# Performance work log

Measured on AMD Instinct MI355X. Metric: run time of the kernel, lower is better.

Reference implementation:

```python
import jax, jax.numpy as jnp
import numpy as np

FRAMES_IN = 5   # SAMPLING_INPUT_FRAMES = 50 // 10
FRAMES_OUT = 3  # SAMPLING_OUTPUT_FRAMES = 30 // 10
T, N, F, C, H = 512, 60, 2, 64, 512  # trajectories, nodes, features, gcn out, lstm hidden
DIST_THRESH = 10.0
EXIST_THRESH = 0.04


def setup_inputs() -> dict:
    key = jax.random.key(0)
    ks = jax.random.split(key, 24)
    p = {}
    p["feature_input"] = jax.random.normal(ks[0], (FRAMES_IN, T * N, F), jnp.float32)
    p["adj"] = jax.random.randint(ks[1], (FRAMES_IN, T, N, N), 0, 2).astype(jnp.float32)
    p["std"] = jax.random.uniform(ks[2], (F,), jnp.float32)
    p["mean"] = jax.random.normal(ks[3], (F,), jnp.float32)
    # GCNConv params
    p["gcn_W"] = jax.random.normal(ks[4], (F, C), jnp.float32) / np.sqrt(F)
    p["gcn_b"] = jnp.zeros((C,), jnp.float32)
    # LSTM params (PyTorch layout: gates i,f,g,o stacked)
    In = C * N
    s = 1.0 / np.sqrt(H)
    p["W_ih"] = jax.random.uniform(ks[5], (4 * H, In), jnp.float32, -s, s)
    p["W_hh"] = jax.random.uniform(ks[6], (4 * H, H), jnp.float32, -s, s)
    p["b_ih"] = jax.random.uniform(ks[7], (4 * H,), jnp.float32, -s, s)
    p["b_hh"] = jax.random.uniform(ks[8], (4 * H,), jnp.float32, -s, s)
    # MLP: H->512->1028->512->F*N
    def lin(k, fi, fo):
        b = 1.0 / np.sqrt(fi)
        return jax.random.uniform(k, (fi, fo), jnp.float32, -b, b)
    p["W1"] = lin(ks[9], H, 512); p["b1"] = jnp.zeros((512,), jnp.float32)
    p["W2"] = lin(ks[10], 512, 1028); p["b2"] = jnp.zeros((1028,), jnp.float32)
    p["W3"] = lin(ks[11], 1028, 512); p["b3"] = jnp.zeros((512,), jnp.float32)
    p["W4"] = lin(ks[12], 512, F * N); p["b4"] = jnp.zeros((F * N,), jnp.float32)
    return p


def _gcn(x_flat, adjf, gcn_W, gcn_b):
    # x_flat: [T*N, F]; adjf: [T, N, N] block-diagonal graph per trajectory
    x = x_flat.reshape(T, N, F)
    A = adjf + jnp.eye(N, dtype=adjf.dtype)  # PyG GCNConv adds self-loops on top
    deg = A.sum(-1)                            # [T, N]
    norm = jnp.where(deg > 0, jax.lax.rsqrt(deg), 0.0)
    h = x @ gcn_W                              # [T, N, C]
    out = norm[..., None] * jnp.einsum('tij,tjc->tic', A, norm[..., None] * h) + gcn_b
    return out.reshape(T, N * C)


def _lstm(x, h, c, W_ih, W_hh, b_ih, b_hh):
    gates = x @ W_ih.T + b_ih + h @ W_hh.T + b_hh
    i, f, g, o = jnp.split(gates, 4, axis=-1)
    c = jax.nn.sigmoid(f) * c + jax.nn.sigmoid(i) * jnp.tanh(g)
    h = jax.nn.sigmoid(o) * jnp.tanh(c)
    return h, c


def _mlp(h, W1, b1, W2, b2, W3, b3, W4, b4):
    h = jax.nn.relu(h @ W1 + b1)
    h = jax.nn.relu(h @ W2 + b2)
    h = jax.nn.relu(h @ W3 + b3)
    return h @ W4 + b4  # [T, F*N]


def _find_adj(pred, std, mean):
    # radius-graph construction (denormalized coords, block per trajectory)
    x = jax.lax.stop_gradient(pred * std + mean).reshape(T, N, F)
    exist = (x[..., 0] > EXIST_THRESH) & (x[..., 1] > EXIST_THRESH)  # [T, N]
    diff = x[:, :, None, :2] - x[:, None, :, :2]
    dist = jnp.sqrt(jnp.sum(diff * diff, -1))                        # [T, N, N]
    eye = jnp.eye(N, dtype=bool)
    conn = ((dist > 0) & (dist < DIST_THRESH)) | eye
    adj = exist[:, :, None] & exist[:, None, :] & conn
    return adj.astype(pred.dtype)


def reference(feature_input, adj, std, mean, gcn_W, gcn_b, W_ih, W_hh, b_ih, b_hh,
              W1, b1, W2, b2, W3, b3, W4, b4):
    h = jnp.zeros((T, H), feature_input.dtype)
    c = jnp.zeros((T, H), feature_input.dtype)
    enc = [feature_input[0]]
    for i in range(FRAMES_IN - 1):  # break at last frame in original
        g = _gcn(feature_input[i], adj[i], gcn_W, gcn_b)
        h, c = _lstm(g, h, c, W_ih, W_hh, b_ih, b_hh)
        pred = _mlp(h, W1, b1, W2, b2, W3, b3, W4, b4).reshape(T * N, F)
        enc.append(pred)
    cur_x, cur_adj = feature_input[FRAMES_IN - 1], adj[FRAMES_IN - 1]
    dec = []
    for _ in range(FRAMES_OUT):
        g = _gcn(cur_x, cur_adj, gcn_W, gcn_b)
        h, c = _lstm(g, h, c, W_ih, W_hh, b_ih, b_hh)
        pred = _mlp(h, W1, b1, W2, b2, W3, b3, W4, b4).reshape(T * N, F)
        dec.append(pred)
        cur_x = pred
        cur_adj = _find_adj(pred, std, mean)
    return jnp.stack(enc), jnp.stack(dec)
```

## Files before the change

### kernel.cpp

```cpp
#include <hip/hip_runtime.h>

#define T_ 512
#define N_ 60
#define F_ 2
#define C_ 64
#define H_ 512
#define IN_ 3840
#define FOURH 2048
#define PRED_SZ 61440
#define ADJ_SZ 1843200
#define K2_ 128
#define LDSK 40
#define HSLOT 262144

typedef __attribute__((ext_vector_type(8))) short bf8;
typedef __attribute__((ext_vector_type(4))) float f4;

__device__ __forceinline__ unsigned short f2bf(float f)
{
    unsigned int u = __float_as_uint(f);
    u = (u + 0x7FFFu + ((u >> 16) & 1u)) >> 16;
    return (unsigned short)u;
}

__global__ void prep_init_k(const float* Whh, const float* W1, const float* W2,
                            const float* W3, const float* W4, const float* feat,
                            unsigned short* Whh_bf, unsigned short* W1_bf,
                            unsigned short* W2_bf, unsigned short* W3_bf,
                            unsigned short* W4_bf,
                            unsigned short* hAll, float* c, float* out)
{
    long i = (long)blockIdx.x * 256 + threadIdx.x;
    if (i < 1048576) { Whh_bf[i] = f2bf(Whh[i]); return; }
    i -= 1048576;
    if (i < 262144) { W1_bf[i] = f2bf(W1[i]); return; }
    i -= 262144;
    if (i < 526336) { W2_bf[i] = f2bf(W2[i]); return; }
    i -= 526336;
    if (i < 526336) { W3_bf[i] = f2bf(W3[i]); return; }
    i -= 526336;
    if (i < 61440) { W4_bf[i] = f2bf(W4[i]); return; }
    i -= 61440;
    hAll[i] = 0;
    c[i] = 0.0f;
    if (i < PRED_SZ) out[i] = feat[i];
}

__global__ __launch_bounds__(256) void wih2_k(
    const float* Wih, const float* W, const float* b,
    const float* bih, const float* bhh,
    unsigned short* Wih2_bf, float* biasAll)
{
    __shared__ float row[IN_];
    __shared__ float wc[2][64];
    __shared__ float bb[64];
    __shared__ float red[256];

    int o = blockIdx.x;
    int tid = threadIdx.x;

    if (tid < 128) wc[tid >> 6][tid & 63] = W[tid];
    if (tid < 64) bb[tid] = b[tid];
    for (int k = tid; k < IN_; k += 256) row[k] = Wih[(long)o * IN_ + k];
    __syncthreads();

    if (tid < 128) {
        float s = 0.0f;
        if (tid < 120) {
            int n = tid >> 1;
            int f = tid & 1;
            for (int c2 = 0; c2 < 64; ++c2) s += row[n * 64 + c2] * wc[f][c2];
        }
        Wih2_bf[(long)o * K2_ + tid] = f2bf(s);
    }

    float sb = 0.0f;
    for (int k = tid; k < IN_; k += 256) sb += row[k] * bb[k & 63];
    red[tid] = sb;
    __syncthreads();
    for (int s = 128; s > 0; s >>= 1) {
        if (tid < s) red[tid] += red[tid + s];
        __syncthreads();
    }
    if (tid == 0) biasAll[o] = bih[o] + bhh[o] + red[0];
}

__global__ __launch_bounds__(128) void gcn_enc_y(
    const float* x, const float* adj, unsigned short* Y)
{
    __shared__ float sA[N_][N_];
    __shared__ float sx[N_][2];
    __shared__ float snorm[N_];

    int frame = blockIdx.x >> 9;
    int t = blockIdx.x & 511;
    const float* xf = x + (long)frame * PRED_SZ + (long)t * 120;
    const float* af = adj + (long)frame * ADJ_SZ + (long)t * 3600;
    int tid = threadIdx.x;

    for (int l = tid; l < N_ * N_; l += 128) {
        int i = l / N_;
        int j = l - i * N_;
        float a = af[l];
        if (i == j) a += 1.0f;
        sA[i][j] = a;
    }
    if (tid < 120) sx[tid >> 1][tid & 1] = xf[tid];
    __syncthreads();

    if (tid < N_) {
        float d = 0.0f;
        for (int j = 0; j < N_; ++j) d += sA[tid][j];
        snorm[tid] = (d > 0.0f) ? rsqrtf(d) : 0.0f;
    }
    __syncthreads();

    if (tid < 128) {
        float y = 0.0f;
        if (tid < 120) {
            int n = tid >> 1;
            int f = tid & 1;
            float s = 0.0f;
            for (int j = 0; j < N_; ++j) s += sA[n][j] * snorm[j] * sx[j][f];
            y = snorm[n] * s;
        }
        Y[(long)blockIdx.x * K2_ + tid] = f2bf(y);
    }
}

__global__ __launch_bounds__(128) void gcn_dec_y(
    const float* pred, const float* stdv, const float* meanv, unsigned short* Y)
{
    __shared__ float sA[N_][N_];
    __shared__ float sx[N_][2];
    __shared__ float dx0[N_];
    __shared__ float dx1[N_];
    __shared__ int sex[N_];
    __shared__ float snorm[N_];

    int t = blockIdx.x;
    int tid = threadIdx.x;
    const float* pr = pred + (long)t * 120;

    if (tid < 120) sx[tid >> 1][tid & 1] = pr[tid];
    if (tid < N_) {
        float vx = pr[tid * 2 + 0] * stdv[0] + meanv[0];
        float vy = pr[tid * 2 + 1] * stdv[1] + meanv[1];
        dx0[tid] = vx;
        dx1[tid] = vy;
        sex[tid] = (vx > 0.04f) && (vy > 0.04f);
    }
    __syncthreads();

    for (int l = tid; l < N_ * N_; l += 128) {
        int i = l / N_;
        int j = l - i * N_;
        float ddx = dx0[i] - dx0[j];
        float ddy = dx1[i] - dx1[j];
        float d = sqrtf(ddx * ddx + ddy * ddy);
        int conn = ((d > 0.0f) && (d < 10.0f)) || (i == j);
        float a = (sex[i] && sex[j] && conn) ? 1.0f : 0.0f;
        if (i == j) a += 1.0f;
        sA[i][j] = a;
    }
    __syncthreads();

    if (tid < N_) {
        float d = 0.0f;
        for (int j = 0; j < N_; ++j) d += sA[tid][j];
        snorm[tid] = (d > 0.0f) ? rsqrtf(d) : 0.0f;
    }
    __syncthreads();

    if (tid < 128) {
        float y = 0.0f;
        if (tid < 120) {
            int n = tid >> 1;
            int f = tid & 1;
            float s = 0.0f;
            for (int j = 0; j < N_; ++j) s += sA[n][j] * snorm[j] * sx[j][f];
            y = snorm[n] * s;
        }
        Y[(long)t * K2_ + tid] = f2bf(y);
    }
}

__global__ __launch_bounds__(256) void mlp_gemm(
    const unsigned short* Abf, const unsigned short* Bb,
    const float* bias1, float* Cf, unsigned short* Cbf,
    int M, int Nc, int K, int mode)
{
    __shared__ unsigned short As[2][32 * LDSK];
    __shared__ unsigned short Bs[2][32 * LDSK];

    int tid = threadIdx.x;
    int wave = tid >> 6;
    int wt = wave >> 1, wj = wave & 1;
    int lane = tid & 63;
    int quad = lane >> 4;
    int l16 = lane & 15;
    int row0 = blockIdx.y * 32;
    int col0 = blockIdx.x * 32;

    f4 acc = {0.f, 0.f, 0.f, 0.f};
    const ushort4 zu = make_ushort4(0, 0, 0, 0);

    int sr = tid >> 3;
    int sko = (tid & 7) * 4;

    auto loadA = [&](int k0, ushort4& v) {
        int gm = row0 + sr, gk = k0 + sko;
        v = zu;
        if (gm < M && gk + 4 <= K) v = *(const ushort4*)&Abf[(long)gm * K + gk];
    };
    auto loadB = [&](int k0, ushort4& v) {
        int gk = k0 + sr;
        int gn0 = col0 + sko;
        v = zu;
        if (gk < K) {
            if (gn0 + 4 <= Nc) {
                v = *(const ushort4*)&Bb[(long)gk * Nc + gn0];
            } else {
                unsigned short tmp[4] = {0, 0, 0, 0};
                for (int i = 0; i < 4; ++i)
                    if (gn0 + i < Nc) tmp[i] = Bb[(long)gk * Nc + gn0 + i];
                v = make_ushort4(tmp[0], tmp[1], tmp[2], tmp[3]);
            }
        }
    };

    int niter = (K + 31) / 32;
    ushort4 a0, b0, a1 = zu, b1 = zu, a2 = zu, b2 = zu;
    loadA(0, a0);
    loadB(0, b0);
    if (niter > 1) { loadA(32, a1); loadB(32, b1); }

    for (int it = 0; it < niter; ++it) {
        if (it + 2 < niter) {
            loadA((it + 2) * 32, a2);
            loadB((it + 2) * 32, b2);
        }
        int bf = it & 1;
        *(ushort4*)&As[bf][sr * LDSK + sko] = a0;
        Bs[bf][(sko + 0) * LDSK + sr] = b0.x;
        Bs[bf][(sko + 1) * LDSK + sr] = b0.y;
        Bs[bf][(sko + 2) * LDSK + sr] = b0.z;
        Bs[bf][(sko + 3) * LDSK + sr] = b0.w;
        __syncthreads();

        bf8 fa = *(const bf8*)&As[bf][(wt * 16 + l16) * LDSK + quad * 8];
        bf8 fb = *(const bf8*)&Bs[bf][(wj * 16 + l16) * LDSK + quad * 8];
        acc = __builtin_amdgcn_mfma_f32_16x16x32_bf16(fa, fb, acc, 0, 0, 0);

        a0 = a1; a1 = a2; b0 = b1; b1 = b2;
    }

    int gn = col0 + wj * 16 + l16;
    if (gn < Nc) {
        float bsv = bias1[gn];
        #pragma unroll
        for (int r = 0; r < 4; ++r) {
            int gm = row0 + wt * 16 + quad * 4 + r;
            if (gm >= M) continue;
            float v = acc[r] + bsv;
            long idx = (long)gm * Nc + gn;
            if (mode == 2) {
                if (v < 0.0f) v = 0.0f;
                Cbf[idx] = f2bf(v);
            } else {
                Cf[idx] = v;
            }
        }
    }
}

__global__ __launch_bounds__(256) void mlp_w1b(
    const unsigned short* hAll, const unsigned short* Bb,
    const float* bias1, unsigned short* Cbf)
{
    __shared__ unsigned short As[2][32 * LDSK];
    __shared__ unsigned short Bs[2][32 * LDSK];

    int tid = threadIdx.x;
    int wave = tid >> 6;
    int wt = wave >> 1, wj = wave & 1;
    int lane = tid & 63;
    int quad = lane >> 4;
    int l16 = lane & 15;
    int row0 = blockIdx.y * 32;
    int col0 = blockIdx.x * 32;

    f4 acc = {0.f, 0.f, 0.f, 0.f};
    int sr = tid >> 3;
    int sko = (tid & 7) * 4;

    int gr = row0 + sr;
    int sidx = gr >> 9;
    int slot = (sidx < 4) ? (sidx + 1) : 7;
    const unsigned short* arow = hAll + (long)slot * HSLOT + (long)(gr & 511) * H_;

    auto loadA = [&](int k0, ushort4& v) {
        v = *(const ushort4*)&arow[k0 + sko];
    };
    auto loadB = [&](int k0, ushort4& v) {
        v = *(const ushort4*)&Bb[(long)(k0 + sr) * 512 + col0 + sko];
    };

    ushort4 a0, b0, a1, b1, a2 = make_ushort4(0,0,0,0), b2 = a2;
    loadA(0, a0); loadB(0, b0);
    loadA(32, a1); loadB(32, b1);

    for (int it = 0; it < 16; ++it) {
        if (it + 2 < 16) { loadA((it + 2) * 32, a2); loadB((it + 2) * 32, b2); }
        int bf = it & 1;
        *(ushort4*)&As[bf][sr * LDSK + sko] = a0;
        Bs[bf][(sko + 0) * LDSK + sr] = b0.x;
        Bs[bf][(sko + 1) * LDSK + sr] = b0.y;
        Bs[bf][(sko + 2) * LDSK + sr] = b0.z;
        Bs[bf][(sko + 3) * LDSK + sr] = b0.w;
        __syncthreads();

        bf8 fa = *(const bf8*)&As[bf][(wt * 16 + l16) * LDSK + quad * 8];
        bf8 fb = *(const bf8*)&Bs[bf][(wj * 16 + l16) * LDSK + quad * 8];
        acc = __builtin_amdgcn_mfma_f32_16x16x32_bf16(fa, fb, acc, 0, 0, 0);

        a0 = a1; a1 = a2; b0 = b1; b1 = b2;
    }

    int gn = col0 + wj * 16 + l16;
    float bsv = bias1[gn];
    #pragma unroll
    for (int r = 0; r < 4; ++r) {
        int gm = row0 + wt * 16 + quad * 4 + r;
        float v = acc[r] + bsv;
        if (v < 0.0f) v = 0.0f;
        Cbf[(long)gm * 512 + gn] = f2bf(v);
    }
}

__global__ __launch_bounds__(256) void mlp_w4b(
    const unsigned short* Abf, const unsigned short* Bb,
    const float* bias1, float* out)
{
    __shared__ unsigned short As[2][32 * LDSK];
    __shared__ unsigned short Bs[2][32 * LDSK];

    int tid = threadIdx.x;
    int wave = tid >> 6;
    int wt = wave >> 1, wj = wave & 1;
    int lane = tid & 63;
    int quad = lane >> 4;
    int l16 = lane & 15;
    int row0 = blockIdx.y * 32;
    int col0 = blockIdx.x * 32;

    f4 acc = {0.f, 0.f, 0.f, 0.f};
    const ushort4 zu = make_ushort4(0, 0, 0, 0);
    int sr = tid >> 3;
    int sko = (tid & 7) * 4;

    auto loadA = [&](int k0, ushort4& v) {
        v = *(const ushort4*)&Abf[(long)(row0 + sr) * 512 + k0 + sko];
    };
    auto loadB = [&](int k0, ushort4& v) {
        int gn0 = col0 + sko;
        v = zu;
        if (gn0 + 4 <= 120) {
            v = *(const ushort4*)&Bb[(long)(k0 + sr) * 120 + gn0];
        } else {
            unsigned short tmp[4] = {0, 0, 0, 0};
            for (int i = 0; i < 4; ++i)
                if (gn0 + i < 120) tmp[i] = Bb[(long)(k0 + sr) * 120 + gn0 + i];
            v = make_ushort4(tmp[0], tmp[1], tmp[2], tmp[3]);
        }
    };

    ushort4 a0, b0, a1, b1, a2 = zu, b2 = zu;
    loadA(0, a0); loadB(0, b0);
    loadA(32, a1); loadB(32, b1);

    for (int it = 0; it < 16; ++it) {
        if (it + 2 < 16) { loadA((it + 2) * 32, a2); loadB((it + 2) * 32, b2); }
        int bf = it & 1;
        *(ushort4*)&As[bf][sr * LDSK + sko] = a0;
        Bs[bf][(sko + 0) * LDSK + sr] = b0.x;
        Bs[bf][(sko + 1) * LDSK + sr] = b0.y;
        Bs[bf][(sko + 2) * LDSK + sr] = b0.z;
        Bs[bf][(sko + 3) * LDSK + sr] = b0.w;
        __syncthreads();

        bf8 fa = *(const bf8*)&As[bf][(wt * 16 + l16) * LDSK + quad * 8];
        bf8 fb = *(const bf8*)&Bs[bf][(wj * 16 + l16) * LDSK + quad * 8];
        acc = __builtin_amdgcn_mfma_f32_16x16x32_bf16(fa, fb, acc, 0, 0, 0);

        a0 = a1; a1 = a2; b0 = b1; b1 = b2;
    }

    int gn = col0 + wj * 16 + l16;
    if (gn < 120) {
        float bsv = bias1[gn];
        #pragma unroll
        for (int r = 0; r < 4; ++r) {
            int gm = row0 + wt * 16 + quad * 4 + r;
            int sidx = gm >> 9;
            int frame = (sidx < 4) ? (sidx + 1) : 7;
            out[(long)frame * PRED_SZ + (long)(gm & 511) * 120 + gn] = acc[r] + bsv;
        }
    }
}

__global__ __launch_bounds__(256) void whh_lstm_k(
    const unsigned short* hprev, const unsigned short* Whh_bf,
    const unsigned short* Yf, const unsigned short* Wih2_bf,
    const float* biasAll, float* c, unsigned short* hnew)
{
    __shared__ unsigned short As[2][32 * LDSK];
    __shared__ unsigned short Bs[2][128 * LDSK];

    int tid = threadIdx.x;
    int wave = tid >> 6;
    int wt = wave >> 1, wj = wave & 1;
    int lane = tid & 63;
    int quad = lane >> 4;
    int l16 = lane & 15;
    int j0 = blockIdx.x * 32;
    int row0 = blockIdx.y * 32;

    int sr = tid >> 3;
    int sko = (tid & 7) * 4;
    int br = tid >> 1;
    int bko = (tid & 1) * 16;
    long brow = (long)((br >> 5) * H_ + j0 + (br & 31));
    long bb_w = brow * H_;
    long bb_y = brow * K2_;
    long ar_h = (long)(row0 + sr) * H_;
    long ar_y = (long)(row0 + sr) * K2_;

    f4 acc[4];
    #pragma unroll
    for (int g = 0; g < 4; ++g) acc[g] = f4{0.f, 0.f, 0.f, 0.f};

    auto loadT = [&](int it, ushort4& a, uint4& q0, uint4& q1) {
        if (it < 4) {
            int k = it * 32;
            a  = *(const ushort4*)&Yf[ar_y + k + sko];
            q0 = *(const uint4*)&Wih2_bf[bb_y + k + bko];
            q1 = *(const uint4*)&Wih2_bf[bb_y + k + bko + 8];
        } else {
            int k = (it - 4) * 32;
            a  = *(const ushort4*)&hprev[ar_h + k + sko];
            q0 = *(const uint4*)&Whh_bf[bb_w + k + bko];
            q1 = *(const uint4*)&Whh_bf[bb_w + k + bko + 8];
        }
    };

    ushort4 a0, a1, a2 = make_ushort4(0, 0, 0, 0);
    uint4 q00, q01, q10, q11, q20 = uint4{0,0,0,0}, q21 = uint4{0,0,0,0};
    loadT(0, a0, q00, q01);
    loadT(1, a1, q10, q11);

    for (int it = 0; it < 20; ++it) {
        if (it + 2 < 20) loadT(it + 2, a2, q20, q21);
        int bf = it & 1;
        *(ushort4*)&As[bf][sr * LDSK + sko] = a0;
        *(uint4*)&Bs[bf][br * LDSK + bko]     = q00;
        *(uint4*)&Bs[bf][br * LDSK + bko + 8] = q01;
        __syncthreads();

        bf8 fa = *(const bf8*)&As[bf][(wt * 16 + l16) * LDSK + quad * 8];
        #pragma unroll
        for (int g = 0; g < 4; ++g) {
            bf8 fb = *(const bf8*)&Bs[bf][(g * 32 + wj * 16 + l16) * LDSK + quad * 8];
            acc[g] = __builtin_amdgcn_mfma_f32_16x16x32_bf16(fa, fb, acc[g], 0, 0, 0);
        }

        a0 = a1; a1 = a2;
        q00 = q10; q01 = q11; q10 = q20; q11 = q21;
    }

    int j = j0 + wj * 16 + l16;
    float b_i = biasAll[j];
    float b_f = biasAll[512 + j];
    float b_g = biasAll[1024 + j];
    float b_o = biasAll[1536 + j];
    #pragma unroll
    for (int r = 0; r < 4; ++r) {
        int t = row0 + wt * 16 + quad * 4 + r;
        float gi = acc[0][r] + b_i;
        float gf = acc[1][r] + b_f;
        float gg = acc[2][r] + b_g;
        float go = acc[3][r] + b_o;
        float ig = 1.0f / (1.0f + expf(-gi));
        float fg = 1.0f / (1.0f + expf(-gf));
        float g2 = tanhf(gg);
        float og = 1.0f / (1.0f + expf(-go));
        long ci = (long)t * H_ + j;
        float cn = fg * c[ci] + ig * g2;
        c[ci] = cn;
        hnew[ci] = f2bf(og * tanhf(cn));
    }
}

extern "C" void kernel_launch(void* const* d_in, const int* in_sizes, int n_in,
                              void* d_out, int out_size, void* d_ws, size_t ws_size,
                              hipStream_t stream)
{
    const float* feat  = (const float*)d_in[0];
    const float* adjin = (const float*)d_in[1];
    const float* stdv  = (const float*)d_in[2];
    const float* meanv = (const float*)d_in[3];
    const float* gcnW  = (const float*)d_in[4];
    const float* gcnb  = (const float*)d_in[5];
    const float* Wih   = (const float*)d_in[6];
    const float* Whh   = (const float*)d_in[7];
    const float* bih   = (const float*)d_in[8];
    const float* bhh   = (const float*)d_in[9];
    const float* W1    = (const float*)d_in[10];
    const float* b1    = (const float*)d_in[11];
    const float* W2    = (const float*)d_in[12];
    const float* b2    = (const float*)d_in[13];
    const float* W3    = (const float*)d_in[14];
    const float* b3    = (const float*)d_in[15];
    const float* W4    = (const float*)d_in[16];
    const float* b4    = (const float*)d_in[17];
    float* out = (float*)d_out;

    float* c       = (float*)d_ws;
    float* biasAll = c + 262144;
    unsigned short* Y       = (unsigned short*)(biasAll + 2048);
    unsigned short* hAll    = Y + 5 * 65536;
    unsigned short* m1      = hAll + 8 * HSLOT;
    unsigned short* m2      = m1 + 1310720;
    unsigned short* m3      = m2 + 2631680;
    unsigned short* Whh_bf  = m3 + 1310720;
    unsigned short* W1_bf   = Whh_bf + 1048576;
    unsigned short* W2_bf   = W1_bf + 262144;
    unsigned short* W3_bf   = W2_bf + 526336;
    unsigned short* W4_bf   = W3_bf + 526336;
    unsigned short* Wih2_bf = W4_bf + 61440;

    prep_init_k<<<10496, 256, 0, stream>>>(Whh, W1, W2, W3, W4, feat,
                                           Whh_bf, W1_bf, W2_bf, W3_bf, W4_bf,
                                           hAll, c, out);
    wih2_k<<<FOURH, 256, 0, stream>>>(Wih, gcnW, gcnb, bih, bhh, Wih2_bf, biasAll);
    gcn_enc_y<<<5 * T_, 128, 0, stream>>>(feat, adjin, Y);

    for (int s = 0; s < 5; ++s)
        whh_lstm_k<<<dim3(16, 16), 256, 0, stream>>>(hAll + (long)s * HSLOT,
                                                     Whh_bf, Y + (long)s * 65536,
                                                     Wih2_bf, biasAll, c,
                                                     hAll + (long)(s + 1) * HSLOT);

    for (int s = 4; s <= 5; ++s) {
        const unsigned short* hs = hAll + (long)(s + 1) * HSLOT;
        mlp_gemm<<<dim3(16, 16), 256, 0, stream>>>(hs, W1_bf, b1,
                                                   (float*)0, m1, T_, 512, 512, 2);
        mlp_gemm<<<dim3(33, 16), 256, 0, stream>>>(m1, W2_bf, b2,
                                                   (float*)0, m2, T_, 1028, 512, 2);
        mlp_gemm<<<dim3(16, 16), 256, 0, stream>>>(m2, W3_bf, b3,
                                                   (float*)0, m3, T_, 512, 1028, 2);
        mlp_gemm<<<dim3(4, 16), 256, 0, stream>>>(m3, W4_bf, b4,
                                                  out + (long)(s + 1) * PRED_SZ,
                                                  (unsigned short*)0, T_, 120, 512, 3);
        gcn_dec_y<<<T_, 128, 0, stream>>>(out + (long)(s + 1) * PRED_SZ,
                                          stdv, meanv, Y);
        whh_lstm_k<<<dim3(16, 16), 256, 0, stream>>>(hAll + (long)(s + 1) * HSLOT,
                                                     Whh_bf, Y, Wih2_bf, biasAll, c,
                                                     hAll + (long)(s + 2) * HSLOT);
    }

    mlp_w1b<<<dim3(16, 80), 256, 0, stream>>>(hAll, W1_bf, b1, m1);
    mlp_gemm<<<dim3(33, 80), 256, 0, stream>>>(m1, W2_bf, b2,
                                               (float*)0, m2, 2560, 1028, 512, 2);
    mlp_gemm<<<dim3(16, 80), 256, 0, stream>>>(m2, W3_bf, b3,
                                               (float*)0, m3, 2560, 512, 1028, 2);
    mlp_w4b<<<dim3(4, 80), 256, 0, stream>>>(m3, W4_bf, b4, out);
}
```

Before: 374.4 us.

## Fuse sequential LSTM/MLP/GCN chain into one cooperative persistent kernel

Replaces the long chain of small dependent launches (5 encoder LSTM steps, then the decoder MLP, GCN and LSTM steps) with a single cooperative kernel of 256 blocks. The stages are separated by grid.sync instead of kernel boundaries. This is meant to remove per-launch overhead and idle gaps between many tiny kernels. The decoder GCN input gets its own Ydec buffer, and the old multi-launch path remains as a fallback if the cooperative launch fails. The trade-offs are grid-wide barrier cost and a single fixed tiling for every phase.

```diff
diff --git a/kernel.cpp b/kernel.cpp
--- a/kernel.cpp
+++ b/kernel.cpp
@@ -1,4 +1,7 @@
 #include <hip/hip_runtime.h>
+#include <hip/hip_cooperative_groups.h>
+
+namespace cg = cooperative_groups;
 
 #define T_ 512
 #define N_ 60
@@ -204,7 +207,6 @@
 
     f4 acc = {0.f, 0.f, 0.f, 0.f};
     const ushort4 zu = make_ushort4(0, 0, 0, 0);
-
     int sr = tid >> 3;
     int sko = (tid & 7) * 4;
 
@@ -501,6 +503,304 @@
     }
 }
 
+
+__device__ __forceinline__ void whh_phase(
+    unsigned char* smem, int tid, int blk,
+    const unsigned short* hprev, const unsigned short* Whh_bf,
+    const unsigned short* Yf, const unsigned short* Wih2_bf,
+    const float* biasAll, float* c, unsigned short* hnew, int withH)
+{
+    unsigned short* AsB = (unsigned short*)smem;
+    unsigned short* BsB = (unsigned short*)(smem + 5120);
+
+    int wave = tid >> 6;
+    int wt = wave >> 1, wj = wave & 1;
+    int lane = tid & 63;
+    int quad = lane >> 4;
+    int l16 = lane & 15;
+    int j0 = (blk & 15) * 32;
+    int row0 = (blk >> 4) * 32;
+
+    int sr = tid >> 3;
+    int sko = (tid & 7) * 4;
+    int br = tid >> 1;
+    int bko = (tid & 1) * 16;
+    long brow = (long)((br >> 5) * H_ + j0 + (br & 31));
+    long bb_w = brow * H_;
+    long bb_y = brow * K2_;
+    long ar_h = (long)(row0 + sr) * H_;
+    long ar_y = (long)(row0 + sr) * K2_;
+
+    f4 acc[4];
+    #pragma unroll
+    for (int g = 0; g < 4; ++g) acc[g] = f4{0.f, 0.f, 0.f, 0.f};
+
+    int niter = withH ? 20 : 4;
+
+    auto loadT = [&](int it, ushort4& a, uint4& q0, uint4& q1) {
+        if (it < 4) {
+            int k = it * 32;
+            a  = *(const ushort4*)&Yf[ar_y + k + sko];
+            q0 = *(const uint4*)&Wih2_bf[bb_y + k + bko];
+            q1 = *(const uint4*)&Wih2_bf[bb_y + k + bko + 8];
+        } else {
+            int k = (it - 4) * 32;
+            a  = *(const ushort4*)&hprev[ar_h + k + sko];
+            q0 = *(const uint4*)&Whh_bf[bb_w + k + bko];
+            q1 = *(const uint4*)&Whh_bf[bb_w + k + bko + 8];
+        }
+    };
+
+    ushort4 a0, a1, a2 = make_ushort4(0, 0, 0, 0);
+    uint4 q00, q01, q10, q11, q20 = uint4{0,0,0,0}, q21 = uint4{0,0,0,0};
+    loadT(0, a0, q00, q01);
+    loadT(1, a1, q10, q11);
+
+    for (int it = 0; it < niter; ++it) {
+        if (it + 2 < niter) loadT(it + 2, a2, q20, q21);
+        int bf = it & 1;
+        *(ushort4*)&AsB[bf * 1280 + sr * LDSK + sko] = a0;
+        *(uint4*)&BsB[bf * 5120 + br * LDSK + bko]     = q00;
+        *(uint4*)&BsB[bf * 5120 + br * LDSK + bko + 8] = q01;
+        __syncthreads();
+
+        bf8 fa = *(const bf8*)&AsB[bf * 1280 + (wt * 16 + l16) * LDSK + quad * 8];
+        #pragma unroll
+        for (int g = 0; g < 4; ++g) {
+            bf8 fb = *(const bf8*)&BsB[bf * 5120 + (g * 32 + wj * 16 + l16) * LDSK + quad * 8];
+            acc[g] = __builtin_amdgcn_mfma_f32_16x16x32_bf16(fa, fb, acc[g], 0, 0, 0);
+        }
+
+        a0 = a1; a1 = a2;
+        q00 = q10; q01 = q11; q10 = q20; q11 = q21;
+    }
+
+    int j = j0 + wj * 16 + l16;
+    float b_i = biasAll[j];
+    float b_f = biasAll[512 + j];
+    float b_g = biasAll[1024 + j];
+    float b_o = biasAll[1536 + j];
+    #pragma unroll
+    for (int r = 0; r < 4; ++r) {
+        int t = row0 + wt * 16 + quad * 4 + r;
+        float gi = acc[0][r] + b_i;
+        float gf = acc[1][r] + b_f;
+        float gg = acc[2][r] + b_g;
+        float go = acc[3][r] + b_o;
+        float ig = 1.0f / (1.0f + expf(-gi));
+        float fg = 1.0f / (1.0f + expf(-gf));
+        float g2 = tanhf(gg);
+        float og = 1.0f / (1.0f + expf(-go));
+        long ci = (long)t * H_ + j;
+        float cn = fg * c[ci] + ig * g2;
+        c[ci] = cn;
+        hnew[ci] = f2bf(og * tanhf(cn));
+    }
+}
+
+__device__ __forceinline__ void mlp_phase(
+    unsigned char* smem, int tid, int blk, int nblk,
+    const unsigned short* Abf, const unsigned short* Bb,
+    const float* bias1, float* Cf, unsigned short* Cbf,
+    int M, int Nc, int K, int mode)
+{
+    unsigned short* AsB = (unsigned short*)smem;
+    unsigned short* BsB = (unsigned short*)(smem + 5120);
+
+    int wave = tid >> 6;
+    int wt = wave >> 1, wj = wave & 1;
+    int lane = tid & 63;
+    int quad = lane >> 4;
+    int l16 = lane & 15;
+    int sr = tid >> 3;
+    int sko = (tid & 7) * 4;
+    const ushort4 zu = make_ushort4(0, 0, 0, 0);
+
+    int ntx = (Nc + 31) >> 5;
+    int NT = ntx * ((M + 31) >> 5);
+    int niter = (K + 31) / 32;
+
+    for (int tile = blk; tile < NT; tile += nblk) {
+        int col0 = (tile % ntx) * 32;
+        int row0 = (tile / ntx) * 32;
+
+        f4 acc = {0.f, 0.f, 0.f, 0.f};
+
+        auto loadA = [&](int k0, ushort4& v) {
+            int gm = row0 + sr, gk = k0 + sko;
+            v = zu;
+            if (gm < M && gk + 4 <= K) v = *(const ushort4*)&Abf[(long)gm * K + gk];
+        };
+        auto loadB = [&](int k0, ushort4& v) {
+            int gk = k0 + sr;
+            int gn0 = col0 + sko;
+            v = zu;
+            if (gk < K) {
+                if (gn0 + 4 <= Nc) {
+                    v = *(const ushort4*)&Bb[(long)gk * Nc + gn0];
+                } else {
+                    unsigned short tmp[4] = {0, 0, 0, 0};
+                    for (int i = 0; i < 4; ++i)
+                        if (gn0 + i < Nc) tmp[i] = Bb[(long)gk * Nc + gn0 + i];
+                    v = make_ushort4(tmp[0], tmp[1], tmp[2], tmp[3]);
+                }
+            }
+        };
+
+        ushort4 a0, b0, a1 = zu, b1 = zu, a2 = zu, b2 = zu;
+        loadA(0, a0);
+        loadB(0, b0);
+        if (niter > 1) { loadA(32, a1); loadB(32, b1); }
+
+        for (int it = 0; it < niter; ++it) {
+            if (it + 2 < niter) {
+                loadA((it + 2) * 32, a2);
+                loadB((it + 2) * 32, b2);
+            }
+            int bf = it & 1;
+            *(ushort4*)&AsB[bf * 1280 + sr * LDSK + sko] = a0;
+            BsB[bf * 1280 + (sko + 0) * LDSK + sr] = b0.x;
+            BsB[bf * 1280 + (sko + 1) * LDSK + sr] = b0.y;
+            BsB[bf * 1280 + (sko + 2) * LDSK + sr] = b0.z;
+            BsB[bf * 1280 + (sko + 3) * LDSK + sr] = b0.w;
+            __syncthreads();
+
+            bf8 fa = *(const bf8*)&AsB[bf * 1280 + (wt * 16 + l16) * LDSK + quad * 8];
+            bf8 fb = *(const bf8*)&BsB[bf * 1280 + (wj * 16 + l16) * LDSK + quad * 8];
+            acc = __builtin_amdgcn_mfma_f32_16x16x32_bf16(fa, fb, acc, 0, 0, 0);
+
+            a0 = a1; a1 = a2; b0 = b1; b1 = b2;
+        }
+
+        int gn = col0 + wj * 16 + l16;
+        if (gn < Nc) {
+            float bsv = bias1[gn];
+            #pragma unroll
+            for (int r = 0; r < 4; ++r) {
+                int gm = row0 + wt * 16 + quad * 4 + r;
+                if (gm >= M) continue;
+                float v = acc[r] + bsv;
+                long idx = (long)gm * Nc + gn;
+                if (mode == 2) {
+                    if (v < 0.0f) v = 0.0f;
+                    Cbf[idx] = f2bf(v);
+                } else {
+                    Cf[idx] = v;
+                }
+            }
+        }
+        __syncthreads();
+    }
+}
+
+__device__ __forceinline__ void gcn_phase(
+    unsigned char* smem, int tid, int blk,
+    const float* pred, const float* stdv, const float* meanv,
+    unsigned short* Y)
+{
+    int half = tid >> 7;
+    int lt = tid & 127;
+    int t = blk * 2 + half;
+
+    float* sA    = (float*)(smem + half * 15872);
+    float* sx    = sA + 3600;
+    float* dx0   = sx + 120;
+    float* dx1   = dx0 + 60;
+    int*   sex   = (int*)(dx1 + 60);
+    float* snorm = (float*)(sex + 60);
+
+    const float* pr = pred + (long)t * 120;
+
+    if (lt < 120) sx[lt] = pr[lt];
+    if (lt < N_) {
+        float vx = pr[lt * 2 + 0] * stdv[0] + meanv[0];
+        float vy = pr[lt * 2 + 1] * stdv[1] + meanv[1];
+        dx0[lt] = vx;
+        dx1[lt] = vy;
+        sex[lt] = (vx > 0.04f) && (vy > 0.04f);
+    }
+    __syncthreads();
+
+    for (int l = lt; l < N_ * N_; l += 128) {
+        int i = l / N_;
+        int j = l - i * N_;
+        float ddx = dx0[i] - dx0[j];
+        float ddy = dx1[i] - dx1[j];
+        float d = sqrtf(ddx * ddx + ddy * ddy);
+        int conn = ((d > 0.0f) && (d < 10.0f)) || (i == j);
+        float a = (sex[i] && sex[j] && conn) ? 1.0f : 0.0f;
+        if (i == j) a += 1.0f;
+        sA[l] = a;
+    }
+    __syncthreads();
+
+    if (lt < N_) {
+        float d = 0.0f;
+        for (int j = 0; j < N_; ++j) d += sA[lt * N_ + j];
+        snorm[lt] = (d > 0.0f) ? rsqrtf(d) : 0.0f;
+    }
+    __syncthreads();
+
+    {
+        float y = 0.0f;
+        if (lt < 120) {
+            int n = lt >> 1;
+            int f = lt & 1;
+            float s = 0.0f;
+            for (int j = 0; j < N_; ++j) s += sA[n * N_ + j] * snorm[j] * sx[j * 2 + f];
+            y = snorm[n] * s;
+        }
+        Y[(long)t * K2_ + lt] = f2bf(y);
+    }
+    __syncthreads();
+}
+
+__global__ void __launch_bounds__(256) spine_k(
+    const unsigned short* Whh_bf, const unsigned short* Wih2_bf,
+    const float* biasAll, float* c, unsigned short* hAll,
+    const unsigned short* Yenc, unsigned short* Ydec,
+    const unsigned short* W1_bf, const float* b1,
+    const unsigned short* W2_bf, const float* b2,
+    const unsigned short* W3_bf, const float* b3,
+    const unsigned short* W4_bf, const float* b4,
+    unsigned short* m1, unsigned short* m2, unsigned short* m3,
+    float* out, const float* stdv, const float* meanv)
+{
+    cg::grid_group grid = cg::this_grid();
+    __shared__ __align__(16) unsigned char smem[31744];
+    int tid = threadIdx.x;
+    int blk = blockIdx.x;
+
+    for (int s = 0; s < 5; ++s) {
+        whh_phase(smem, tid, blk, hAll + (long)s * HSLOT, Whh_bf,
+                  Yenc + (long)s * 65536, Wih2_bf, biasAll, c,
+                  hAll + (long)(s + 1) * HSLOT, s > 0);
+        grid.sync();
+    }
+
+    for (int s = 4; s <= 5; ++s) {
+        const unsigned short* hs = hAll + (long)(s + 1) * HSLOT;
+        mlp_phase(smem, tid, blk, 256, hs, W1_bf, b1, (float*)0, m1,
+                  512, 512, 512, 2);
+        grid.sync();
+        mlp_phase(smem, tid, blk, 256, m1, W2_bf, b2, (float*)0, m2,
+                  512, 1028, 512, 2);
+        grid.sync();
+        mlp_phase(smem, tid, blk, 256, m2, W3_bf, b3, (float*)0, m3,
+                  512, 512, 1028, 2);
+        grid.sync();
+        mlp_phase(smem, tid, blk, 256, m3, W4_bf, b4,
+                  out + (long)(s + 1) * PRED_SZ, (unsigned short*)0,
+                  512, 120, 512, 3);
+        grid.sync();
+        gcn_phase(smem, tid, blk, out + (long)(s + 1) * PRED_SZ, stdv, meanv, Ydec);
+        grid.sync();
+        whh_phase(smem, tid, blk, hAll + (long)(s + 1) * HSLOT, Whh_bf,
+                  Ydec, Wih2_bf, biasAll, c, hAll + (long)(s + 2) * HSLOT, 1);
+        if (s == 4) grid.sync();
+    }
+}
+
 extern "C" void kernel_launch(void* const* d_in, const int* in_sizes, int n_in,
                               void* d_out, int out_size, void* d_ws, size_t ws_size,
                               hipStream_t stream)
@@ -528,7 +828,8 @@
     float* c       = (float*)d_ws;
     float* biasAll = c + 262144;
     unsigned short* Y       = (unsigned short*)(biasAll + 2048);
-    unsigned short* hAll    = Y + 5 * 65536;
+    unsigned short* Ydec    = Y + 5 * 65536;
+    unsigned short* hAll    = Y + 6 * 65536;
     unsigned short* m1      = hAll + 8 * HSLOT;
     unsigned short* m2      = m1 + 1310720;
     unsigned short* m3      = m2 + 2631680;
@@ -545,28 +846,49 @@
     wih2_k<<<FOURH, 256, 0, stream>>>(Wih, gcnW, gcnb, bih, bhh, Wih2_bf, biasAll);
     gcn_enc_y<<<5 * T_, 128, 0, stream>>>(feat, adjin, Y);
 
-    for (int s = 0; s < 5; ++s)
-        whh_lstm_k<<<dim3(16, 16), 256, 0, stream>>>(hAll + (long)s * HSLOT,
-                                                     Whh_bf, Y + (long)s * 65536,
-                                                     Wih2_bf, biasAll, c,
-                                                     hAll + (long)(s + 1) * HSLOT);
-
-    for (int s = 4; s <= 5; ++s) {
-        const unsigned short* hs = hAll + (long)(s + 1) * HSLOT;
-        mlp_gemm<<<dim3(16, 16), 256, 0, stream>>>(hs, W1_bf, b1,
-                                                   (float*)0, m1, T_, 512, 512, 2);
-        mlp_gemm<<<dim3(33, 16), 256, 0, stream>>>(m1, W2_bf, b2,
-                                                   (float*)0, m2, T_, 1028, 512, 2);
-        mlp_gemm<<<dim3(16, 16), 256, 0, stream>>>(m2, W3_bf, b3,
-                                                   (float*)0, m3, T_, 512, 1028, 2);
-        mlp_gemm<<<dim3(4, 16), 256, 0, stream>>>(m3, W4_bf, b4,
-                                                  out + (long)(s + 1) * PRED_SZ,
-                                                  (unsigned short*)0, T_, 120, 512, 3);
-        gcn_dec_y<<<T_, 128, 0, stream>>>(out + (long)(s + 1) * PRED_SZ,
-                                          stdv, meanv, Y);
-        whh_lstm_k<<<dim3(16, 16), 256, 0, stream>>>(hAll + (long)(s + 1) * HSLOT,
-                                                     Whh_bf, Y, Wih2_bf, biasAll, c,
-                                                     hAll + (long)(s + 2) * HSLOT);
+    const unsigned short* Whh_c = Whh_bf;
+    const unsigned short* Wih2_c = Wih2_bf;
+    const float* biasAll_c = biasAll;
+    const unsigned short* Yenc_c = Y;
+    const unsigned short* W1c = W1_bf; const unsigned short* W2c = W2_bf;
+    const unsigned short* W3c = W3_bf; const unsigned short* W4c = W4_bf;
+    const float* b1c = b1; const float* b2c = b2;
+    const float* b3c = b3; const float* b4c = b4;
+    const float* stdc = stdv; const float* meanc = meanv;
+    void* kargs[] = {
+        (void*)&Whh_c, (void*)&Wih2_c, (void*)&biasAll_c, (void*)&c, (void*)&hAll,
+        (void*)&Yenc_c, (void*)&Ydec,
+        (void*)&W1c, (void*)&b1c, (void*)&W2c, (void*)&b2c,
+        (void*)&W3c, (void*)&b3c, (void*)&W4c, (void*)&b4c,
+        (void*)&m1, (void*)&m2, (void*)&m3,
+        (void*)&out, (void*)&stdc, (void*)&meanc
+    };
+    hipError_t cerr = hipLaunchCooperativeKernel((const void*)spine_k,
+                                                 dim3(256), dim3(256),
+                                                 kargs, 0u, stream);
+    if (cerr != hipSuccess) {
+        for (int s = 0; s < 5; ++s)
+            whh_lstm_k<<<dim3(16, 16), 256, 0, stream>>>(hAll + (long)s * HSLOT,
+                                                         Whh_bf, Y + (long)s * 65536,
+                                                         Wih2_bf, biasAll, c,
+                                                         hAll + (long)(s + 1) * HSLOT);
+        for (int s = 4; s <= 5; ++s) {
+            const unsigned short* hs = hAll + (long)(s + 1) * HSLOT;
+            mlp_gemm<<<dim3(16, 16), 256, 0, stream>>>(hs, W1_bf, b1,
+                                                       (float*)0, m1, T_, 512, 512, 2);
+            mlp_gemm<<<dim3(33, 16), 256, 0, stream>>>(m1, W2_bf, b2,
+                                                       (float*)0, m2, T_, 1028, 512, 2);
+            mlp_gemm<<<dim3(16, 16), 256, 0, stream>>>(m2, W3_bf, b3,
+                                                       (float*)0, m3, T_, 512, 1028, 2);
+            mlp_gemm<<<dim3(4, 16), 256, 0, stream>>>(m3, W4_bf, b4,
+                                                      out + (long)(s + 1) * PRED_SZ,
+                                                      (unsigned short*)0, T_, 120, 512, 3);
+            gcn_dec_y<<<T_, 128, 0, stream>>>(out + (long)(s + 1) * PRED_SZ,
+                                              stdv, meanv, Ydec);
+            whh_lstm_k<<<dim3(16, 16), 256, 0, stream>>>(hAll + (long)(s + 1) * HSLOT,
+                                                         Whh_bf, Ydec, Wih2_bf, biasAll, c,
+                                                         hAll + (long)(s + 2) * HSLOT);
+        }
     }
 
     mlp_w1b<<<dim3(16, 80), 256, 0, stream>>>(hAll, W1_bf, b1, m1);
```

After: 852.9 us. +127.8%, slower.
